# Performance work log

Hardware: AMD Instinct MI355X
Metric: run time of the kernel (lower is better)

## Reference

```python
import jax, jax.numpy as jnp
import numpy as np

B, T, F = 4096, 512, 8
U1, U2, DH = 8, 16, 16  # GRU1 units, GRU2 units, dense hidden


def _gru(x, W, Uw, b, units):
    """Keras GRU (v2, reset_after=True), activation=relu, recurrent_activation=sigmoid.
    x: [B, T, F_in]; W: [F_in, 3u]; Uw: [u, 3u]; b: [2, 3u]. Returns [B, T, u]."""
    bi, br = b[0], b[1]
    # precompute input projections for all timesteps: [T, B, 3u] (time-major for scan)
    gx = jnp.einsum('btf,fg->tbg', x, W) + bi
    u = units

    def step(h, xt):
        inner = h @ Uw + br                      # [B, 3u]
        z = jax.nn.sigmoid(xt[:, :u] + inner[:, :u])
        r = jax.nn.sigmoid(xt[:, u:2 * u] + inner[:, u:2 * u])
        hh = jax.nn.relu(xt[:, 2 * u:] + r * inner[:, 2 * u:])
        h = z * h + (1.0 - z) * hh
        return h, h

    h0 = jnp.zeros((x.shape[0], u), dtype=x.dtype)
    _, ys = jax.lax.scan(step, h0, gx)           # ys: [T, B, u]
    return jnp.transpose(ys, (1, 0, 2))          # [B, T, u]


def setup_inputs() -> dict:
    key = jax.random.key(0)
    ks = jax.random.split(key, 12)
    s = lambda fan_in: 1.0 / np.sqrt(fan_in)
    x = jax.random.normal(ks[0], (B, T, F), dtype=jnp.float32)
    W1 = jax.random.normal(ks[1], (F, 3 * U1), dtype=jnp.float32) * s(F)
    Ur1 = jax.random.normal(ks[2], (U1, 3 * U1), dtype=jnp.float32) * s(U1)
    b1 = jnp.zeros((2, 3 * U1), dtype=jnp.float32)
    W2 = jax.random.normal(ks[3], (U1, 3 * U2), dtype=jnp.float32) * s(U1)
    Ur2 = jax.random.normal(ks[4], (U2, 3 * U2), dtype=jnp.float32) * s(U2)
    b2 = jnp.zeros((2, 3 * U2), dtype=jnp.float32)
    Wd = jax.random.normal(ks[5], (U2, DH), dtype=jnp.float32) * 0.05  # random_normal init
    bd = jnp.zeros((DH,), dtype=jnp.float32)
    Wo = jax.random.normal(ks[6], (DH, 1), dtype=jnp.float32) * s(DH)
    bo = jnp.zeros((1,), dtype=jnp.float32)
    return {"x": x, "W1": W1, "Ur1": Ur1, "b1": b1, "W2": W2, "Ur2": Ur2,
            "b2": b2, "Wd": Wd, "bd": bd, "Wo": Wo, "bo": bo}


def reference(x, W1, Ur1, b1, W2, Ur2, b2, Wd, bd, Wo, bo):
    # Dropout layers are identity at inference (training=False)
    h = _gru(x, W1, Ur1, b1, U1)                 # [B, T, 8]
    h = _gru(h, W2, Ur2, b2, U2)                 # [B, T, 16]
    h = jax.nn.relu(h @ Wd + bd)                 # [B, T, 16]
    out = h @ Wo + bo                            # [B, T, 1]
    return out
```

## Files before the change

### kernel.cpp

```cpp
#include <hip/hip_runtime.h>

#define TT 512
#define CH 32
#define NCH 16
#define NPH (NCH + 2)
#define LOG2E 1.44269504088896340736f

typedef float f2 __attribute__((ext_vector_type(2)));

template <int N>
__device__ __forceinline__ int rorki_(int v) {
    return __builtin_amdgcn_update_dpp(v, v, 0x120 + N, 0xf, 0xf, true);
}
template <int N>
__device__ __forceinline__ float rorkf_(float v) { return __int_as_float(rorki_<N>(__float_as_int(v))); }
template <int C>
__device__ __forceinline__ float shrf_(float v) {
    return __int_as_float(__builtin_amdgcn_update_dpp(0, __float_as_int(v), C, 0xf, 0xf, true));
}
__device__ __forceinline__ float sgm_(float v) {
    return __builtin_amdgcn_rcpf(1.f + __builtin_amdgcn_exp2f(-v));
}
__device__ __forceinline__ f2 pfma_(f2 a, f2 b, f2 c) {
    return __builtin_elementwise_fma(a, b, c);
}

__launch_bounds__(128)
__attribute__((amdgpu_waves_per_eu(2, 2)))
__global__ void gru_ws(const float* __restrict__ x,
                       const float* __restrict__ W1, const float* __restrict__ Ur1,
                       const float* __restrict__ b1,
                       const float* __restrict__ W2, const float* __restrict__ Ur2,
                       const float* __restrict__ b2,
                       const float* __restrict__ Wd, const float* __restrict__ bd,
                       const float* __restrict__ Wo, const float* __restrict__ bo,
                       float* __restrict__ out)
{
    __shared__ float h1b[2][CH][4][8];
    __shared__ float h2b[2][CH][4][16];

    const int tid  = threadIdx.x;
    const int wv   = tid >> 6;
    const int lane = tid & 63;
    const int g    = lane >> 4;
    const int j    = lane & 15;
    const int u1   = j & 7;
    const int hi   = j >> 3;
    const int gcol = u1 + 8 * hi;
    const bool ishi = (hi != 0);
    const bool isw  = (j == 15);

    int Lk[16];
    Lk[0]  = j;
    Lk[1]  = rorki_<1>(j);   Lk[2]  = rorki_<2>(j);   Lk[3]  = rorki_<3>(j);
    Lk[4]  = rorki_<4>(j);   Lk[5]  = rorki_<5>(j);   Lk[6]  = rorki_<6>(j);
    Lk[7]  = rorki_<7>(j);   Lk[8]  = rorki_<8>(j);   Lk[9]  = rorki_<9>(j);
    Lk[10] = rorki_<10>(j);  Lk[11] = rorki_<11>(j);  Lk[12] = rorki_<12>(j);
    Lk[13] = rorki_<13>(j);  Lk[14] = rorki_<14>(j);  Lk[15] = rorki_<15>(j);

    if (wv == 0) {
        f2 Gx[4], Hx[4], VC[4], VQ[4];
#pragma unroll
        for (int k = 0; k < 4; ++k) {
            const int a = Lk[2 * k] & 7, b = Lk[2 * k + 1] & 7;
            Gx[k] = f2{LOG2E * W1[a * 24 + gcol],  LOG2E * W1[b * 24 + gcol]};
            Hx[k] = f2{W1[a * 24 + 16 + u1],       W1[b * 24 + 16 + u1]};
            VC[k] = f2{LOG2E * Ur1[a * 24 + gcol], LOG2E * Ur1[b * 24 + gcol]};
            VQ[k] = f2{Ur1[a * 24 + 16 + u1],      Ur1[b * 24 + 16 + u1]};
        }
        f2 Pd[8];
#pragma unroll
        for (int k = 0; k < 8; ++k)
            Pd[k] = f2{Wd[(2 * k) * 16 + j], Wd[(2 * k + 1) * 16 + j]};
        const float bAzr = LOG2E * (b1[gcol] + b1[24 + gcol]);
        const float bGh  = b1[16 + u1];
        const float bIh  = b1[40 + u1];
        const float bdj  = bd[j], woj = Wo[j], boo = bo[0];

        const float* xbase = x + (size_t)blockIdx.x * 4 * TT * 8;
        const int    xoff  = g * TT * 8 + u1;
        float* outrow = out + (size_t)(blockIdx.x * 4 + g) * TT;

        float h1own = 0.f, azrP = bAzr, ihP = bIh;
        float xA = xbase[0 * 8 + xoff];
        float xB = xbase[1 * 8 + xoff];
        float xC = xbase[2 * 8 + xoff];
        float4 hA0, hA1, hA2, hA3, hB0, hB1, hB2, hB3;

#define G1STEP(TG, SL, XCUR, XFILL)                                          \
    {                                                                        \
        const float x0 = XCUR;                                               \
        const f2 xp0 = f2{x0,            rorkf_<1>(x0)};                     \
        const f2 xp1 = f2{rorkf_<2>(x0), rorkf_<3>(x0)};                     \
        const f2 xp2 = f2{rorkf_<4>(x0), rorkf_<5>(x0)};                     \
        const f2 xp3 = f2{rorkf_<6>(x0), rorkf_<7>(x0)};                     \
        f2 axp = f2{azrP, 0.f}, ghp = f2{bGh, 0.f};                          \
        axp = pfma_(xp0, Gx[0], axp);  ghp = pfma_(xp0, Hx[0], ghp);         \
        axp = pfma_(xp1, Gx[1], axp);  ghp = pfma_(xp1, Hx[1], ghp);         \
        axp = pfma_(xp2, Gx[2], axp);  ghp = pfma_(xp2, Hx[2], ghp);         \
        axp = pfma_(xp3, Gx[3], axp);  ghp = pfma_(xp3, Hx[3], ghp);         \
        XFILL = xbase[(((TG) + 3) & (TT - 1)) * 8 + xoff];                   \
        const float azrC = axp.x + axp.y;                                    \
        const float s_own = sgm_(azrC);                                      \
        const float s_sw  = rorkf_<8>(s_own);                                \
        const float z1 = ishi ? s_sw : s_own;                                \
        const float r1 = ishi ? s_own : s_sw;                                \
        const float hh1 = fmaxf(fmaf(r1, ihP, ghp.x + ghp.y), 0.f);          \
        h1own = fmaf(z1, h1own - hh1, hh1);                                  \
        const float n0 = h1own;                                              \
        const f2 np0 = f2{n0,            rorkf_<1>(n0)};                     \
        const f2 np1 = f2{rorkf_<2>(n0), rorkf_<3>(n0)};                     \
        const f2 np2 = f2{rorkf_<4>(n0), rorkf_<5>(n0)};                     \
        const f2 np3 = f2{rorkf_<6>(n0), rorkf_<7>(n0)};                     \
        f2 aNp = f2{bAzr, 0.f}, iNp = f2{bIh, 0.f};                          \
        aNp = pfma_(np0, VC[0], aNp);  iNp = pfma_(np0, VQ[0], iNp);         \
        aNp = pfma_(np1, VC[1], aNp);  iNp = pfma_(np1, VQ[1], iNp);         \
        aNp = pfma_(np2, VC[2], aNp);  iNp = pfma_(np2, VQ[2], iNp);         \
        aNp = pfma_(np3, VC[3], aNp);  iNp = pfma_(np3, VQ[3], iNp);         \
        azrP = aNp.x + aNp.y;  ihP = iNp.x + iNp.y;                          \
        h1b[p & 1][SL][g][u1] = h1own;                                       \
    }

#define DSTEP(DL, C0, C1, C2, C3, N0, N1, N2, N3, DN)                        \
    {                                                                        \
        f2 da = f2{bdj, 0.f};                                                \
        da = pfma_(f2{C0.x, C0.y}, Pd[0], da);                               \
        da = pfma_(f2{C0.z, C0.w}, Pd[1], da);                               \
        da = pfma_(f2{C1.x, C1.y}, Pd[2], da);                               \
        da = pfma_(f2{C1.z, C1.w}, Pd[3], da);                               \
        da = pfma_(f2{C2.x, C2.y}, Pd[4], da);                               \
        da = pfma_(f2{C2.z, C2.w}, Pd[5], da);                               \
        da = pfma_(f2{C3.x, C3.y}, Pd[6], da);                               \
        da = pfma_(f2{C3.z, C3.w}, Pd[7], da);                               \
        N0 = *(const float4*)&h2b[p & 1][DN][g][0];                          \
        N1 = *(const float4*)&h2b[p & 1][DN][g][4];                          \
        N2 = *(const float4*)&h2b[p & 1][DN][g][8];                          \
        N3 = *(const float4*)&h2b[p & 1][DN][g][12];                         \
        float e = fmaxf(da.x + da.y, 0.f) * woj;                             \
        e += shrf_<0x118>(e);                                                \
        e += shrf_<0x114>(e);                                                \
        e += shrf_<0x112>(e);                                                \
        e += shrf_<0x111>(e);                                                \
        if (isw) outd[DL] = e + boo;                                         \
    }

        for (int p = 0; p < NPH; ++p) {
            if (p < 2) {
                const int t0 = p * CH;
                for (int s = 0; s < CH; s += 4) {
                    G1STEP(t0 + s + 0, s + 0, xA, xA)
                    G1STEP(t0 + s + 1, s + 1, xB, xB)
                    G1STEP(t0 + s + 2, s + 2, xC, xC)
                    G1STEP(t0 + s + 3, s + 3, xA, xA)
                    { float t = xB; xB = xC; xC = xA; xA = t; }
                }
            } else if (p < NCH) {
                const int t0 = p * CH;
                float* outd = outrow + (p - 2) * CH;
                hA0 = *(const float4*)&h2b[p & 1][0][g][0];
                hA1 = *(const float4*)&h2b[p & 1][0][g][4];
                hA2 = *(const float4*)&h2b[p & 1][0][g][8];
                hA3 = *(const float4*)&h2b[p & 1][0][g][12];
                for (int s = 0; s < CH; s += 4) {
                    G1STEP(t0 + s + 0, s + 0, xA, xA)
                    DSTEP(s + 0, hA0, hA1, hA2, hA3, hB0, hB1, hB2, hB3, s + 1)
                    G1STEP(t0 + s + 1, s + 1, xB, xB)
                    DSTEP(s + 1, hB0, hB1, hB2, hB3, hA0, hA1, hA2, hA3, s + 2)
                    G1STEP(t0 + s + 2, s + 2, xC, xC)
                    DSTEP(s + 2, hA0, hA1, hA2, hA3, hB0, hB1, hB2, hB3, s + 3)
                    G1STEP(t0 + s + 3, s + 3, xA, xA)
                    DSTEP(s + 3, hB0, hB1, hB2, hB3, hA0, hA1, hA2, hA3, (s + 4) & (CH - 1))
                    { float t = xB; xB = xC; xC = xA; xA = t; }
                }
            } else {
                float* outd = outrow + (p - 2) * CH;
                hA0 = *(const float4*)&h2b[p & 1][0][g][0];
                hA1 = *(const float4*)&h2b[p & 1][0][g][4];
                hA2 = *(const float4*)&h2b[p & 1][0][g][8];
                hA3 = *(const float4*)&h2b[p & 1][0][g][12];
                for (int s = 0; s < CH; s += 4) {
                    DSTEP(s + 0, hA0, hA1, hA2, hA3, hB0, hB1, hB2, hB3, s + 1)
                    DSTEP(s + 1, hB0, hB1, hB2, hB3, hA0, hA1, hA2, hA3, s + 2)
                    DSTEP(s + 2, hA0, hA1, hA2, hA3, hB0, hB1, hB2, hB3, s + 3)
                    DSTEP(s + 3, hB0, hB1, hB2, hB3, hA0, hA1, hA2, hA3, (s + 4) & (CH - 1))
                }
            }
            __syncthreads();
        }
#undef G1STEP
#undef DSTEP
    } else {
        f2 Pz[8], Pr[8], Ph[8];
#pragma unroll
        for (int k = 0; k < 8; ++k) {
            const int a = Lk[2 * k], b = Lk[2 * k + 1];
            Pz[k] = f2{LOG2E * Ur2[a * 48 + j],      LOG2E * Ur2[b * 48 + j]};
            Pr[k] = f2{LOG2E * Ur2[a * 48 + 16 + j], LOG2E * Ur2[b * 48 + 16 + j]};
            Ph[k] = f2{Ur2[a * 48 + 32 + j],         Ur2[b * 48 + 32 + j]};
        }
        f2 Vz[4], Vr[4], Vh[4];
#pragma unroll
        for (int k = 0; k < 4; ++k) {
            Vz[k] = f2{LOG2E * W2[(2 * k) * 48 + j],      LOG2E * W2[(2 * k + 1) * 48 + j]};
            Vr[k] = f2{LOG2E * W2[(2 * k) * 48 + 16 + j], LOG2E * W2[(2 * k + 1) * 48 + 16 + j]};
            Vh[k] = f2{W2[(2 * k) * 48 + 32 + j],         W2[(2 * k + 1) * 48 + 32 + j]};
        }
        const float bA2 = LOG2E * (b2[j] + b2[48 + j]);
        const float bB2 = LOG2E * (b2[16 + j] + b2[64 + j]);
        const float bC2 = b2[80 + j];
        const float bD2 = b2[32 + j];

        float h2own = 0.f;
        float4 kA0, kA1, kB0, kB1;

#define G2STEP(SL, K0, K1, M0, M1, SN)                                       \
    {                                                                        \
        const float h0 = h2own;                                              \
        const f2 tp0 = f2{h0,             rorkf_<1>(h0)};                    \
        const f2 tp1 = f2{rorkf_<2>(h0),  rorkf_<3>(h0)};                    \
        const f2 tp2 = f2{rorkf_<4>(h0),  rorkf_<5>(h0)};                    \
        const f2 tp3 = f2{rorkf_<6>(h0),  rorkf_<7>(h0)};                    \
        const f2 tp4 = f2{rorkf_<8>(h0),  rorkf_<9>(h0)};                    \
        const f2 tp5 = f2{rorkf_<10>(h0), rorkf_<11>(h0)};                   \
        const f2 tp6 = f2{rorkf_<12>(h0), rorkf_<13>(h0)};                   \
        const f2 tp7 = f2{rorkf_<14>(h0), rorkf_<15>(h0)};                   \
        f2 za = f2{bA2, 0.f}, ra = f2{bB2, 0.f}, ha = f2{bC2, 0.f};          \
        za = pfma_(tp0, Pz[0], za); ra = pfma_(tp0, Pr[0], ra); ha = pfma_(tp0, Ph[0], ha); \
        za = pfma_(tp1, Pz[1], za); ra = pfma_(tp1, Pr[1], ra); ha = pfma_(tp1, Ph[1], ha); \
        za = pfma_(tp2, Pz[2], za); ra = pfma_(tp2, Pr[2], ra); ha = pfma_(tp2, Ph[2], ha); \
        za = pfma_(tp3, Pz[3], za); ra = pfma_(tp3, Pr[3], ra); ha = pfma_(tp3, Ph[3], ha); \
        za = pfma_(tp4, Pz[4], za); ra = pfma_(tp4, Pr[4], ra); ha = pfma_(tp4, Ph[4], ha); \
        za = pfma_(tp5, Pz[5], za); ra = pfma_(tp5, Pr[5], ra); ha = pfma_(tp5, Ph[5], ha); \
        za = pfma_(tp6, Pz[6], za); ra = pfma_(tp6, Pr[6], ra); ha = pfma_(tp6, Ph[6], ha); \
        za = pfma_(tp7, Pz[7], za); ra = pfma_(tp7, Pr[7], ra); ha = pfma_(tp7, Ph[7], ha); \
        const f2 q0 = f2{K0.x, K0.y}, q1 = f2{K0.z, K0.w};                   \
        const f2 q2 = f2{K1.x, K1.y}, q3 = f2{K1.z, K1.w};                   \
        f2 hbp = f2{bD2, 0.f};                                               \
        za = pfma_(q0, Vz[0], za); ra = pfma_(q0, Vr[0], ra); hbp = pfma_(q0, Vh[0], hbp); \
        za = pfma_(q1, Vz[1], za); ra = pfma_(q1, Vr[1], ra); hbp = pfma_(q1, Vh[1], hbp); \
        za = pfma_(q2, Vz[2], za); ra = pfma_(q2, Vr[2], ra); hbp = pfma_(q2, Vh[2], hbp); \
        za = pfma_(q3, Vz[3], za); ra = pfma_(q3, Vr[3], ra); hbp = pfma_(q3, Vh[3], hbp); \
        M0 = *(const float4*)&h1b[(p - 1) & 1][SN][g][0];                    \
        M1 = *(const float4*)&h1b[(p - 1) & 1][SN][g][4];                    \
        const float z2 = sgm_(za.x + za.y), r2 = sgm_(ra.x + ra.y);          \
        const float hh2 = fmaxf(fmaf(r2, ha.x + ha.y, hbp.x + hbp.y), 0.f);  \
        h2own = fmaf(z2, h2own - hh2, hh2);                                  \
        h2b[(p - 1) & 1][SL][g][j] = h2own;                                  \
    }

        for (int p = 0; p < NPH; ++p) {
            if (p >= 1 && p <= NCH) {
                kA0 = *(const float4*)&h1b[(p - 1) & 1][0][g][0];
                kA1 = *(const float4*)&h1b[(p - 1) & 1][0][g][4];
                for (int s = 0; s < CH; s += 2) {
                    G2STEP(s + 0, kA0, kA1, kB0, kB1, s + 1)
                    G2STEP(s + 1, kB0, kB1, kA0, kA1, (s + 2) & (CH - 1))
                }
            }
            __syncthreads();
        }
#undef G2STEP
    }
}

extern "C" void kernel_launch(void* const* d_in, const int* in_sizes, int n_in,
                              void* d_out, int out_size, void* d_ws, size_t ws_size,
                              hipStream_t stream) {
    const float* x   = (const float*)d_in[0];
    const float* W1  = (const float*)d_in[1];
    const float* Ur1 = (const float*)d_in[2];
    const float* b1  = (const float*)d_in[3];
    const float* W2  = (const float*)d_in[4];
    const float* Ur2 = (const float*)d_in[5];
    const float* b2  = (const float*)d_in[6];
    const float* Wd  = (const float*)d_in[7];
    const float* bd  = (const float*)d_in[8];
    const float* Wo  = (const float*)d_in[9];
    const float* bo  = (const float*)d_in[10];
    float* out = (float*)d_out;

    dim3 grid(4096 / 4);
    dim3 block(128);
    gru_ws<<<grid, block, 0, stream>>>(x, W1, Ur1, b1, W2, Ur2, b2,
                                       Wd, bd, Wo, bo, out);
}
```

Before: 164.8 us.

## Split GRU pipeline into three warp-specialized waves with input-projection stage

Restructures the warp-specialized kernel from two waves to three. Wave 0 now runs only GRU1. A new third wave computes GRU2's input projection (W2·h1) into a shared buffer and also runs the dense head. Wave 1 runs only the GRU2 recurrence, which shortens the critical serial chain per timestep. Chunk size drops from 32 to 16 to cut pipeline fill latency across the now three-deep schedule. In exchange it adds shared memory traffic, more barrier phases, and a larger block.

```diff
diff --git a/kernel.cpp b/kernel.cpp
--- a/kernel.cpp
+++ b/kernel.cpp
@@ -1,9 +1,9 @@
 #include <hip/hip_runtime.h>
 
 #define TT 512
-#define CH 32
-#define NCH 16
-#define NPH (NCH + 2)
+#define CH 16
+#define NCH 32
+#define NPH (NCH + 3)
 #define LOG2E 1.44269504088896340736f
 
 typedef float f2 __attribute__((ext_vector_type(2)));
@@ -25,9 +25,9 @@
     return __builtin_elementwise_fma(a, b, c);
 }
 
-__launch_bounds__(128)
-__attribute__((amdgpu_waves_per_eu(2, 2)))
-__global__ void gru_ws(const float* __restrict__ x,
+__launch_bounds__(192)
+__attribute__((amdgpu_waves_per_eu(3, 3)))
+__global__ void gru_3w(const float* __restrict__ x,
                        const float* __restrict__ W1, const float* __restrict__ Ur1,
                        const float* __restrict__ b1,
                        const float* __restrict__ W2, const float* __restrict__ Ur2,
@@ -38,6 +38,7 @@
 {
     __shared__ float h1b[2][CH][4][8];
     __shared__ float h2b[2][CH][4][16];
+    __shared__ float w2p[2][3][CH][4][16];
 
     const int tid  = threadIdx.x;
     const int wv   = tid >> 6;
@@ -68,24 +69,17 @@
             VC[k] = f2{LOG2E * Ur1[a * 24 + gcol], LOG2E * Ur1[b * 24 + gcol]};
             VQ[k] = f2{Ur1[a * 24 + 16 + u1],      Ur1[b * 24 + 16 + u1]};
         }
-        f2 Pd[8];
-#pragma unroll
-        for (int k = 0; k < 8; ++k)
-            Pd[k] = f2{Wd[(2 * k) * 16 + j], Wd[(2 * k + 1) * 16 + j]};
         const float bAzr = LOG2E * (b1[gcol] + b1[24 + gcol]);
         const float bGh  = b1[16 + u1];
         const float bIh  = b1[40 + u1];
-        const float bdj  = bd[j], woj = Wo[j], boo = bo[0];
 
         const float* xbase = x + (size_t)blockIdx.x * 4 * TT * 8;
         const int    xoff  = g * TT * 8 + u1;
-        float* outrow = out + (size_t)(blockIdx.x * 4 + g) * TT;
 
         float h1own = 0.f, azrP = bAzr, ihP = bIh;
         float xA = xbase[0 * 8 + xoff];
         float xB = xbase[1 * 8 + xoff];
         float xC = xbase[2 * 8 + xoff];
-        float4 hA0, hA1, hA2, hA3, hB0, hB1, hB2, hB3;
 
 #define G1STEP(TG, SL, XCUR, XFILL)                                          \
     {                                                                        \
@@ -121,6 +115,117 @@
         h1b[p & 1][SL][g][u1] = h1own;                                       \
     }
 
+        for (int p = 0; p < NPH; ++p) {
+            if (p < NCH) {
+                const int t0 = p * CH;
+                for (int s = 0; s < CH; s += 4) {
+                    G1STEP(t0 + s + 0, s + 0, xA, xA)
+                    G1STEP(t0 + s + 1, s + 1, xB, xB)
+                    G1STEP(t0 + s + 2, s + 2, xC, xC)
+                    G1STEP(t0 + s + 3, s + 3, xA, xA)
+                    { float t = xB; xB = xC; xC = xA; xA = t; }
+                }
+            }
+            __syncthreads();
+        }
+#undef G1STEP
+    } else if (wv == 1) {
+        f2 Pz[8], Pr[8], Ph[8];
+#pragma unroll
+        for (int k = 0; k < 8; ++k) {
+            const int a = Lk[2 * k], b = Lk[2 * k + 1];
+            Pz[k] = f2{LOG2E * Ur2[a * 48 + j],      LOG2E * Ur2[b * 48 + j]};
+            Pr[k] = f2{LOG2E * Ur2[a * 48 + 16 + j], LOG2E * Ur2[b * 48 + 16 + j]};
+            Ph[k] = f2{Ur2[a * 48 + 32 + j],         Ur2[b * 48 + 32 + j]};
+        }
+        const float bA2 = LOG2E * (b2[j] + b2[48 + j]);
+        const float bB2 = LOG2E * (b2[16 + j] + b2[64 + j]);
+        const float bC2 = b2[80 + j];
+
+        float h2own = 0.f;
+        float zaPc, raPc, hbPc, zaPn, raPn, hbPn;
+
+#define G2STEP(SL, ZAC, RAC, HBC, ZAN, RAN, HBN, SN)                         \
+    {                                                                        \
+        const float h0 = h2own;                                              \
+        const f2 tp0 = f2{h0,             rorkf_<1>(h0)};                    \
+        const f2 tp1 = f2{rorkf_<2>(h0),  rorkf_<3>(h0)};                    \
+        const f2 tp2 = f2{rorkf_<4>(h0),  rorkf_<5>(h0)};                    \
+        const f2 tp3 = f2{rorkf_<6>(h0),  rorkf_<7>(h0)};                    \
+        const f2 tp4 = f2{rorkf_<8>(h0),  rorkf_<9>(h0)};                    \
+        const f2 tp5 = f2{rorkf_<10>(h0), rorkf_<11>(h0)};                   \
+        const f2 tp6 = f2{rorkf_<12>(h0), rorkf_<13>(h0)};                   \
+        const f2 tp7 = f2{rorkf_<14>(h0), rorkf_<15>(h0)};                   \
+        f2 zaA = f2{bA2, 0.f}, raA = f2{bB2, 0.f}, haA = f2{bC2, 0.f};       \
+        f2 zaB = f2{0.f, 0.f}, raB = f2{0.f, 0.f}, haB = f2{0.f, 0.f};       \
+        zaA = pfma_(tp0, Pz[0], zaA); raA = pfma_(tp0, Pr[0], raA); haA = pfma_(tp0, Ph[0], haA); \
+        zaA = pfma_(tp1, Pz[1], zaA); raA = pfma_(tp1, Pr[1], raA); haA = pfma_(tp1, Ph[1], haA); \
+        zaA = pfma_(tp2, Pz[2], zaA); raA = pfma_(tp2, Pr[2], raA); haA = pfma_(tp2, Ph[2], haA); \
+        zaA = pfma_(tp3, Pz[3], zaA); raA = pfma_(tp3, Pr[3], raA); haA = pfma_(tp3, Ph[3], haA); \
+        zaB = pfma_(tp4, Pz[4], zaB); raB = pfma_(tp4, Pr[4], raB); haB = pfma_(tp4, Ph[4], haB); \
+        zaB = pfma_(tp5, Pz[5], zaB); raB = pfma_(tp5, Pr[5], raB); haB = pfma_(tp5, Ph[5], haB); \
+        zaB = pfma_(tp6, Pz[6], zaB); raB = pfma_(tp6, Pr[6], raB); haB = pfma_(tp6, Ph[6], haB); \
+        zaB = pfma_(tp7, Pz[7], zaB); raB = pfma_(tp7, Pr[7], raB); haB = pfma_(tp7, Ph[7], haB); \
+        ZAN = w2p[par][0][SN][g][j];                                         \
+        RAN = w2p[par][1][SN][g][j];                                         \
+        HBN = w2p[par][2][SN][g][j];                                         \
+        const f2 zs = zaA + zaB, rs = raA + raB, hs = haA + haB;             \
+        const float z2 = sgm_(zs.x + zs.y + ZAC);                            \
+        const float r2 = sgm_(rs.x + rs.y + RAC);                            \
+        const float hh2 = fmaxf(fmaf(r2, hs.x + hs.y, HBC), 0.f);            \
+        h2own = fmaf(z2, h2own - hh2, hh2);                                  \
+        h2b[par][SL][g][j] = h2own;                                          \
+    }
+
+        for (int p = 0; p < NPH; ++p) {
+            if (p >= 2 && p <= NCH + 1) {
+                const int par = (p - 2) & 1;
+                zaPc = w2p[par][0][0][g][j];
+                raPc = w2p[par][1][0][g][j];
+                hbPc = w2p[par][2][0][g][j];
+                for (int s = 0; s < CH; s += 2) {
+                    G2STEP(s + 0, zaPc, raPc, hbPc, zaPn, raPn, hbPn, s + 1)
+                    G2STEP(s + 1, zaPn, raPn, hbPn, zaPc, raPc, hbPc, (s + 2) & (CH - 1))
+                }
+            }
+            __syncthreads();
+        }
+#undef G2STEP
+    } else {
+        f2 Vz[4], Vr[4], Vh[4];
+#pragma unroll
+        for (int k = 0; k < 4; ++k) {
+            Vz[k] = f2{LOG2E * W2[(2 * k) * 48 + j],      LOG2E * W2[(2 * k + 1) * 48 + j]};
+            Vr[k] = f2{LOG2E * W2[(2 * k) * 48 + 16 + j], LOG2E * W2[(2 * k + 1) * 48 + 16 + j]};
+            Vh[k] = f2{W2[(2 * k) * 48 + 32 + j],         W2[(2 * k + 1) * 48 + 32 + j]};
+        }
+        f2 Pd[8];
+#pragma unroll
+        for (int k = 0; k < 8; ++k)
+            Pd[k] = f2{Wd[(2 * k) * 16 + j], Wd[(2 * k + 1) * 16 + j]};
+        const float bD2 = b2[32 + j];
+        const float bdj = bd[j], woj = Wo[j], boo = bo[0];
+        float* outrow = out + (size_t)(blockIdx.x * 4 + g) * TT;
+
+        float4 kA0, kA1, kB0, kB1;
+        float4 hA0, hA1, hA2, hA3, hB0, hB1, hB2, hB3;
+
+#define W2STEP(SL, K0, K1, M0, M1, SN)                                       \
+    {                                                                        \
+        const f2 q0 = f2{K0.x, K0.y}, q1 = f2{K0.z, K0.w};                   \
+        const f2 q2 = f2{K1.x, K1.y}, q3 = f2{K1.z, K1.w};                   \
+        f2 zp = f2{0.f, 0.f}, rp = f2{0.f, 0.f}, hp = f2{bD2, 0.f};          \
+        zp = pfma_(q0, Vz[0], zp); rp = pfma_(q0, Vr[0], rp); hp = pfma_(q0, Vh[0], hp); \
+        zp = pfma_(q1, Vz[1], zp); rp = pfma_(q1, Vr[1], rp); hp = pfma_(q1, Vh[1], hp); \
+        zp = pfma_(q2, Vz[2], zp); rp = pfma_(q2, Vr[2], rp); hp = pfma_(q2, Vh[2], hp); \
+        zp = pfma_(q3, Vz[3], zp); rp = pfma_(q3, Vr[3], rp); hp = pfma_(q3, Vh[3], hp); \
+        M0 = *(const float4*)&h1b[parw][SN][g][0];                           \
+        M1 = *(const float4*)&h1b[parw][SN][g][4];                           \
+        w2p[parw][0][SL][g][j] = zp.x + zp.y;                                \
+        w2p[parw][1][SL][g][j] = rp.x + rp.y;                                \
+        w2p[parw][2][SL][g][j] = hp.x + hp.y;                                \
+    }
+
 #define DSTEP(DL, C0, C1, C2, C3, N0, N1, N2, N3, DN)                        \
     {                                                                        \
         f2 da = f2{bdj, 0.f};                                                \
@@ -132,10 +237,10 @@
         da = pfma_(f2{C2.z, C2.w}, Pd[5], da);                               \
         da = pfma_(f2{C3.x, C3.y}, Pd[6], da);                               \
         da = pfma_(f2{C3.z, C3.w}, Pd[7], da);                               \
-        N0 = *(const float4*)&h2b[p & 1][DN][g][0];                          \
-        N1 = *(const float4*)&h2b[p & 1][DN][g][4];                          \
-        N2 = *(const float4*)&h2b[p & 1][DN][g][8];                          \
-        N3 = *(const float4*)&h2b[p & 1][DN][g][12];                         \
+        N0 = *(const float4*)&h2b[pard][DN][g][0];                           \
+        N1 = *(const float4*)&h2b[pard][DN][g][4];                           \
+        N2 = *(const float4*)&h2b[pard][DN][g][8];                           \
+        N3 = *(const float4*)&h2b[pard][DN][g][12];                          \
         float e = fmaxf(da.x + da.y, 0.f) * woj;                             \
         e += shrf_<0x118>(e);                                                \
         e += shrf_<0x114>(e);                                                \
@@ -145,121 +250,43 @@
     }
 
         for (int p = 0; p < NPH; ++p) {
-            if (p < 2) {
-                const int t0 = p * CH;
-                for (int s = 0; s < CH; s += 4) {
-                    G1STEP(t0 + s + 0, s + 0, xA, xA)
-                    G1STEP(t0 + s + 1, s + 1, xB, xB)
-                    G1STEP(t0 + s + 2, s + 2, xC, xC)
-                    G1STEP(t0 + s + 3, s + 3, xA, xA)
-                    { float t = xB; xB = xC; xC = xA; xA = t; }
-                }
-            } else if (p < NCH) {
-                const int t0 = p * CH;
-                float* outd = outrow + (p - 2) * CH;
-                hA0 = *(const float4*)&h2b[p & 1][0][g][0];
-                hA1 = *(const float4*)&h2b[p & 1][0][g][4];
-                hA2 = *(const float4*)&h2b[p & 1][0][g][8];
-                hA3 = *(const float4*)&h2b[p & 1][0][g][12];
-                for (int s = 0; s < CH; s += 4) {
-                    G1STEP(t0 + s + 0, s + 0, xA, xA)
+            const bool doW = (p >= 1 && p <= NCH);
+            const bool doD = (p >= 3 && p <= NCH + 2);
+            const int parw = (p - 1) & 1;
+            const int pard = (p - 3) & 1;
+            float* outd = outrow + (p - 3) * CH;
+            if (doW) {
+                kA0 = *(const float4*)&h1b[parw][0][g][0];
+                kA1 = *(const float4*)&h1b[parw][0][g][4];
+            }
+            if (doD) {
+                hA0 = *(const float4*)&h2b[pard][0][g][0];
+                hA1 = *(const float4*)&h2b[pard][0][g][4];
+                hA2 = *(const float4*)&h2b[pard][0][g][8];
+                hA3 = *(const float4*)&h2b[pard][0][g][12];
+            }
+            if (doW && doD) {
+                for (int s = 0; s < CH; s += 2) {
+                    W2STEP(s + 0, kA0, kA1, kB0, kB1, s + 1)
                     DSTEP(s + 0, hA0, hA1, hA2, hA3, hB0, hB1, hB2, hB3, s + 1)
-                    G1STEP(t0 + s + 1, s + 1, xB, xB)
-                    DSTEP(s + 1, hB0, hB1, hB2, hB3, hA0, hA1, hA2, hA3, s + 2)
-                    G1STEP(t0 + s + 2, s + 2, xC, xC)
-                    DSTEP(s + 2, hA0, hA1, hA2, hA3, hB0, hB1, hB2, hB3, s + 3)
-                    G1STEP(t0 + s + 3, s + 3, xA, xA)
-                    DSTEP(s + 3, hB0, hB1, hB2, hB3, hA0, hA1, hA2, hA3, (s + 4) & (CH - 1))
-                    { float t = xB; xB = xC; xC = xA; xA = t; }
-                }
-            } else {
-                float* outd = outrow + (p - 2) * CH;
-                hA0 = *(const float4*)&h2b[p & 1][0][g][0];
-                hA1 = *(const float4*)&h2b[p & 1][0][g][4];
-                hA2 = *(const float4*)&h2b[p & 1][0][g][8];
-                hA3 = *(const float4*)&h2b[p & 1][0][g][12];
-                for (int s = 0; s < CH; s += 4) {
+                    W2STEP(s + 1, kB0, kB1, kA0, kA1, (s + 2) & (CH - 1))
+                    DSTEP(s + 1, hB0, hB1, hB2, hB3, hA0, hA1, hA2, hA3, (s + 2) & (CH - 1))
+                }
+            } else if (doW) {
+                for (int s = 0; s < CH; s += 2) {
+                    W2STEP(s + 0, kA0, kA1, kB0, kB1, s + 1)
+                    W2STEP(s + 1, kB0, kB1, kA0, kA1, (s + 2) & (CH - 1))
+                }
+            } else if (doD) {
+                for (int s = 0; s < CH; s += 2) {
                     DSTEP(s + 0, hA0, hA1, hA2, hA3, hB0, hB1, hB2, hB3, s + 1)
-                    DSTEP(s + 1, hB0, hB1, hB2, hB3, hA0, hA1, hA2, hA3, s + 2)
-                    DSTEP(s + 2, hA0, hA1, hA2, hA3, hB0, hB1, hB2, hB3, s + 3)
-                    DSTEP(s + 3, hB0, hB1, hB2, hB3, hA0, hA1, hA2, hA3, (s + 4) & (CH - 1))
+                    DSTEP(s + 1, hB0, hB1, hB2, hB3, hA0, hA1, hA2, hA3, (s + 2) & (CH - 1))
                 }
             }
             __syncthreads();
         }
-#undef G1STEP
+#undef W2STEP
 #undef DSTEP
-    } else {
-        f2 Pz[8], Pr[8], Ph[8];
-#pragma unroll
-        for (int k = 0; k < 8; ++k) {
-            const int a = Lk[2 * k], b = Lk[2 * k + 1];
-            Pz[k] = f2{LOG2E * Ur2[a * 48 + j],      LOG2E * Ur2[b * 48 + j]};
-            Pr[k] = f2{LOG2E * Ur2[a * 48 + 16 + j], LOG2E * Ur2[b * 48 + 16 + j]};
-            Ph[k] = f2{Ur2[a * 48 + 32 + j],         Ur2[b * 48 + 32 + j]};
-        }
-        f2 Vz[4], Vr[4], Vh[4];
-#pragma unroll
-        for (int k = 0; k < 4; ++k) {
-            Vz[k] = f2{LOG2E * W2[(2 * k) * 48 + j],      LOG2E * W2[(2 * k + 1) * 48 + j]};
-            Vr[k] = f2{LOG2E * W2[(2 * k) * 48 + 16 + j], LOG2E * W2[(2 * k + 1) * 48 + 16 + j]};
-            Vh[k] = f2{W2[(2 * k) * 48 + 32 + j],         W2[(2 * k + 1) * 48 + 32 + j]};
-        }
-        const float bA2 = LOG2E * (b2[j] + b2[48 + j]);
-        const float bB2 = LOG2E * (b2[16 + j] + b2[64 + j]);
-        const float bC2 = b2[80 + j];
-        const float bD2 = b2[32 + j];
-
-        float h2own = 0.f;
-        float4 kA0, kA1, kB0, kB1;
-
-#define G2STEP(SL, K0, K1, M0, M1, SN)                                       \
-    {                                                                        \
-        const float h0 = h2own;                                              \
-        const f2 tp0 = f2{h0,             rorkf_<1>(h0)};                    \
-        const f2 tp1 = f2{rorkf_<2>(h0),  rorkf_<3>(h0)};                    \
-        const f2 tp2 = f2{rorkf_<4>(h0),  rorkf_<5>(h0)};                    \
-        const f2 tp3 = f2{rorkf_<6>(h0),  rorkf_<7>(h0)};                    \
-        const f2 tp4 = f2{rorkf_<8>(h0),  rorkf_<9>(h0)};                    \
-        const f2 tp5 = f2{rorkf_<10>(h0), rorkf_<11>(h0)};                   \
-        const f2 tp6 = f2{rorkf_<12>(h0), rorkf_<13>(h0)};                   \
-        const f2 tp7 = f2{rorkf_<14>(h0), rorkf_<15>(h0)};                   \
-        f2 za = f2{bA2, 0.f}, ra = f2{bB2, 0.f}, ha = f2{bC2, 0.f};          \
-        za = pfma_(tp0, Pz[0], za); ra = pfma_(tp0, Pr[0], ra); ha = pfma_(tp0, Ph[0], ha); \
-        za = pfma_(tp1, Pz[1], za); ra = pfma_(tp1, Pr[1], ra); ha = pfma_(tp1, Ph[1], ha); \
-        za = pfma_(tp2, Pz[2], za); ra = pfma_(tp2, Pr[2], ra); ha = pfma_(tp2, Ph[2], ha); \
-        za = pfma_(tp3, Pz[3], za); ra = pfma_(tp3, Pr[3], ra); ha = pfma_(tp3, Ph[3], ha); \
-        za = pfma_(tp4, Pz[4], za); ra = pfma_(tp4, Pr[4], ra); ha = pfma_(tp4, Ph[4], ha); \
-        za = pfma_(tp5, Pz[5], za); ra = pfma_(tp5, Pr[5], ra); ha = pfma_(tp5, Ph[5], ha); \
-        za = pfma_(tp6, Pz[6], za); ra = pfma_(tp6, Pr[6], ra); ha = pfma_(tp6, Ph[6], ha); \
-        za = pfma_(tp7, Pz[7], za); ra = pfma_(tp7, Pr[7], ra); ha = pfma_(tp7, Ph[7], ha); \
-        const f2 q0 = f2{K0.x, K0.y}, q1 = f2{K0.z, K0.w};                   \
-        const f2 q2 = f2{K1.x, K1.y}, q3 = f2{K1.z, K1.w};                   \
-        f2 hbp = f2{bD2, 0.f};                                               \
-        za = pfma_(q0, Vz[0], za); ra = pfma_(q0, Vr[0], ra); hbp = pfma_(q0, Vh[0], hbp); \
-        za = pfma_(q1, Vz[1], za); ra = pfma_(q1, Vr[1], ra); hbp = pfma_(q1, Vh[1], hbp); \
-        za = pfma_(q2, Vz[2], za); ra = pfma_(q2, Vr[2], ra); hbp = pfma_(q2, Vh[2], hbp); \
-        za = pfma_(q3, Vz[3], za); ra = pfma_(q3, Vr[3], ra); hbp = pfma_(q3, Vh[3], hbp); \
-        M0 = *(const float4*)&h1b[(p - 1) & 1][SN][g][0];                    \
-        M1 = *(const float4*)&h1b[(p - 1) & 1][SN][g][4];                    \
-        const float z2 = sgm_(za.x + za.y), r2 = sgm_(ra.x + ra.y);          \
-        const float hh2 = fmaxf(fmaf(r2, ha.x + ha.y, hbp.x + hbp.y), 0.f);  \
-        h2own = fmaf(z2, h2own - hh2, hh2);                                  \
-        h2b[(p - 1) & 1][SL][g][j] = h2own;                                  \
-    }
-
-        for (int p = 0; p < NPH; ++p) {
-            if (p >= 1 && p <= NCH) {
-                kA0 = *(const float4*)&h1b[(p - 1) & 1][0][g][0];
-                kA1 = *(const float4*)&h1b[(p - 1) & 1][0][g][4];
-                for (int s = 0; s < CH; s += 2) {
-                    G2STEP(s + 0, kA0, kA1, kB0, kB1, s + 1)
-                    G2STEP(s + 1, kB0, kB1, kA0, kA1, (s + 2) & (CH - 1))
-                }
-            }
-            __syncthreads();
-        }
-#undef G2STEP
     }
 }
 
@@ -280,7 +307,7 @@
     float* out = (float*)d_out;
 
     dim3 grid(4096 / 4);
-    dim3 block(128);
-    gru_ws<<<grid, block, 0, stream>>>(x, W1, Ur1, b1, W2, Ur2, b2,
+    dim3 block(192);
+    gru_3w<<<grid, block, 0, stream>>>(x, W1, Ur1, b1, W2, Ur2, b2,
                                        Wd, bd, Wo, bo, out);
 }
```

After: 186.8 us. 13.3% more time.
